# Optimization experiments

Hardware: AMD Instinct MI355X
Metric: run time of the kernel (lower is better)

Reference implementation:

```python
import jax, jax.numpy as jnp
import numpy as np


def _linear(x, w, b=None):
    # torch nn.Linear: y = x @ W^T + b, W has shape [out, in]
    y = jnp.einsum('...i,oi->...o', x, w)
    return y if b is None else y + b


def setup_inputs() -> dict:
    key = jax.random.key(0)
    ks = jax.random.split(key, 20)
    B, S = 2048, 128

    def w(k, out_d, in_d):
        bound = 1.0 / np.sqrt(in_d)
        return jax.random.uniform(k, (out_d, in_d), jnp.float32, -bound, bound)

    def bias(k, out_d, in_d):
        bound = 1.0 / np.sqrt(in_d)
        return jax.random.uniform(k, (out_d,), jnp.float32, -bound, bound)

    return {
        'x': jax.random.normal(ks[0], (B, S, 8), jnp.float32),
        'w_fm': w(ks[1], 16, 8),  'b_fm': bias(ks[2], 16, 8),
        'w_c1': w(ks[3], 16, 16), 'b_c1': bias(ks[4], 16, 16),
        'w_p1': w(ks[5], 12, 16), 'b_p1': bias(ks[6], 12, 16),
        'w_c2': w(ks[7], 8, 12),  'b_c2': bias(ks[8], 8, 12),
        'w_p2': w(ks[9], 4, 8),   'b_p2': bias(ks[10], 4, 8),
        'w_c3': w(ks[11], 4, 4),  'b_c3': bias(ks[12], 4, 4),
        'w_q': w(ks[13], 4, 4),
        'w_k': w(ks[14], 4, 4),
        'w_v': w(ks[15], 4, 4),
        'w_fc': w(ks[16], 1, 4),  'b_fc': bias(ks[17], 1, 4),
    }


def reference(x, w_fm, b_fm, w_c1, b_c1, w_p1, b_p1, w_c2, b_c2,
              w_p2, b_p2, w_c3, b_c3, w_q, w_k, w_v, w_fc, b_fc):
    EMBED_DIM = 4
    h = jnp.tanh(_linear(x, w_fm, b_fm))   # [B,S,16]
    h = jnp.tanh(_linear(h, w_c1, b_c1))   # [B,S,16]
    h = jnp.tanh(_linear(h, w_p1, b_p1))   # [B,S,12]
    h = jnp.tanh(_linear(h, w_c2, b_c2))   # [B,S,8]
    h = jnp.tanh(_linear(h, w_p2, b_p2))   # [B,S,4]
    h = jnp.tanh(_linear(h, w_c3, b_c3))   # [B,S,4]
    # self-attention over sequence axis
    q = _linear(h, w_q)                     # [B,S,4]
    k = _linear(h, w_k)
    v = _linear(h, w_v)
    scores = jnp.einsum('bqd,bkd->bqk', q, k) / np.sqrt(EMBED_DIM)
    attn = jax.nn.softmax(scores, axis=-1)  # [B,S,S]
    h = jnp.einsum('bqk,bkd->bqd', attn, v) # [B,S,4]
    out = _linear(h, w_fc, b_fc)            # [B,S,1]
    return jax.nn.sigmoid(out)
```

## Files before the change

### kernel.cpp

```cpp
#include <hip/hip_runtime.h>

#define DEV __device__ __forceinline__

typedef _Float16 h2 __attribute__((ext_vector_type(2)));
typedef float    f2 __attribute__((ext_vector_type(2)));

DEV float fast_rcp(float x) { return __builtin_amdgcn_rcpf(x); }

DEV float fexp2(float x) {
#if __has_builtin(__builtin_amdgcn_exp2f)
    return __builtin_amdgcn_exp2f(x);
#else
    float r; asm("v_exp_f32 %0, %1" : "=v"(r) : "v"(x)); return r;
#endif
}

DEV float dot2acc(h2 a, h2 b, float c) {
#if __has_builtin(__builtin_amdgcn_fdot2)
    return __builtin_amdgcn_fdot2(a, b, c, false);
#else
    return c + (float)a.x * (float)b.x + (float)a.y * (float)b.y;
#endif
}

DEV void pk_fma(f2& acc, f2 w2, f2 in2) {
    asm("v_pk_fma_f32 %0, %1, %2, %0" : "+v"(acc) : "s"(w2), "v"(in2));
}
DEV f2 pk_fma_z(f2 w2, f2 in2) {
    f2 d;
    asm("v_pk_fma_f32 %0, %1, %2, 0 op_sel_hi:[1,1,0]"
        : "=v"(d) : "s"(w2), "v"(in2));
    return d;
}
DEV void pk_fma_bcast(f2& acc, f2 e, f2 du) {
    asm("v_pk_fma_f32 %0, %1, %2, %0 op_sel:[0,0,0] op_sel_hi:[0,1,1]"
        : "+v"(acc) : "v"(e), "v"(du));
}

DEV float fast_tanh_pre(float t) {
    float e = fexp2(t);
    return 1.0f - 2.0f * fast_rcp(e + 1.0f);
}
DEV float fast_sigmoid(float x) {
    return fast_rcp(1.0f + fexp2(x * -1.442695041f));
}

#define TANH_K 2.885390082f

template <int IN, int OUT, bool TANH>
DEV void layer_pk(const float* __restrict__ w, const float* __restrict__ b,
                  float vK, const float (&in)[IN], float (&out)[OUT]) {
    static_assert(IN % 2 == 0, "IN must be even");
    f2 in2[IN / 2];
    #pragma unroll
    for (int ip = 0; ip < IN / 2; ++ip) in2[ip] = f2{in[2 * ip], in[2 * ip + 1]};
    #pragma unroll
    for (int o = 0; o < OUT; ++o) {
        f2 acc = pk_fma_z(*reinterpret_cast<const f2*>(w + o * IN), in2[0]);
        #pragma unroll
        for (int ip = 1; ip < IN / 2; ++ip)
            pk_fma(acc, *reinterpret_cast<const f2*>(w + o * IN + 2 * ip), in2[ip]);
        float s = acc.x + acc.y;
        if (TANH) {
            float bk = b[o] * vK;
            out[o] = fast_tanh_pre(fmaf(s, vK, bk));
        } else {
            out[o] = s;
        }
    }
}

__global__ __launch_bounds__(256)
void qcnn_fused_kernel(const float* __restrict__ x,
                       const float* __restrict__ w_fm, const float* __restrict__ b_fm,
                       const float* __restrict__ w_c1, const float* __restrict__ b_c1,
                       const float* __restrict__ w_p1, const float* __restrict__ b_p1,
                       const float* __restrict__ w_c2, const float* __restrict__ b_c2,
                       const float* __restrict__ w_p2, const float* __restrict__ b_p2,
                       const float* __restrict__ w_c3, const float* __restrict__ b_c3,
                       const float* __restrict__ w_q,  const float* __restrict__ w_k,
                       const float* __restrict__ w_v,
                       const float* __restrict__ w_fc, const float* __restrict__ b_fc,
                       float* __restrict__ out) {
    const int t     = threadIdx.x;
    const int bb    = t >> 7;
    const int tok   = t & 127;
    const int batch = blockIdx.x * 2 + bb;

    __shared__ uint4 kvbuf[2][128];

    const float vK = TANH_K;

    const float* xp = x + ((size_t)batch * 128 + tok) * 8;
    float4 x0 = *reinterpret_cast<const float4*>(xp);
    float4 x1 = *reinterpret_cast<const float4*>(xp + 4);
    float xin[8] = {x0.x, x0.y, x0.z, x0.w, x1.x, x1.y, x1.z, x1.w};

    float h1[16], h2a[16], h3[12], h4[8], h5[4], h6[4];
    layer_pk<8, 16, true>(w_fm, b_fm, vK, xin, h1);
    layer_pk<16, 16, true>(w_c1, b_c1, vK, h1, h2a);
    layer_pk<16, 12, true>(w_p1, b_p1, vK, h2a, h3);
    layer_pk<12, 8, true>(w_c2, b_c2, vK, h3, h4);
    layer_pk<8, 4, true>(w_p2, b_p2, vK, h4, h5);
    layer_pk<4, 4, true>(w_c3, b_c3, vK, h5, h6);

    float qv[4], kk[4];
    layer_pk<4, 4, false>(w_q, nullptr, vK, h6, qv);
    layer_pk<4, 4, false>(w_k, nullptr, vK, h6, kk);

    float wf[4];
    #pragma unroll
    for (int i = 0; i < 4; ++i)
        wf[i] = fmaf(w_fc[0], w_v[0 * 4 + i],
                fmaf(w_fc[1], w_v[1 * 4 + i],
                fmaf(w_fc[2], w_v[2 * 4 + i], w_fc[3] * w_v[3 * 4 + i])));
    float u = fmaf(wf[0], h6[0], fmaf(wf[1], h6[1], fmaf(wf[2], h6[2], wf[3] * h6[3])));

    h2 pk01 = {(_Float16)kk[0], (_Float16)kk[1]};
    h2 pk23 = {(_Float16)kk[2], (_Float16)kk[3]};
    uint4 ent;
    ent.x = __builtin_bit_cast(unsigned, pk01);
    ent.y = __builtin_bit_cast(unsigned, pk23);
    ent.z = __builtin_bit_cast(unsigned, 1.0f);
    ent.w = __builtin_bit_cast(unsigned, u);
    kvbuf[bb][tok] = ent;

    const float QS = 0.7213475204f;
    h2 q01 = {(_Float16)(qv[0] * QS), (_Float16)(qv[1] * QS)};
    h2 q23 = {(_Float16)(qv[2] * QS), (_Float16)(qv[3] * QS)};

    __syncthreads();

    unsigned q01u = __builtin_bit_cast(unsigned, q01);
    unsigned q23u = __builtin_bit_cast(unsigned, q23);
    unsigned q01o = __shfl_xor(q01u, 1);
    unsigned q23o = __shfl_xor(q23u, 1);
    const bool odd = (t & 1);
    h2 q01_r0 = __builtin_bit_cast(h2, odd ? q01o : q01u);
    h2 q23_r0 = __builtin_bit_cast(h2, odd ? q23o : q23u);
    h2 q01_r1 = __builtin_bit_cast(h2, odd ? q01u : q01o);
    h2 q23_r1 = __builtin_bit_cast(h2, odd ? q23u : q23o);

    const uint4* __restrict__ base = kvbuf[bb] + (odd ? 64 : 0);
    f2 acc0 = {0.f, 0.f};
    f2 acc1 = {0.f, 0.f};
    #pragma unroll 8
    for (int j = 0; j < 64; ++j) {
        uint4 c = base[j];
        h2 k01 = __builtin_bit_cast(h2, c.x);
        h2 k23 = __builtin_bit_cast(h2, c.y);
        f2 du;
        du.x = __builtin_bit_cast(float, c.z);
        du.y = __builtin_bit_cast(float, c.w);
        float s0 = dot2acc(q01_r0, k01, dot2acc(q23_r0, k23, 0.f));
        float s1 = dot2acc(q01_r1, k01, dot2acc(q23_r1, k23, 0.f));
        f2 e0; e0.x = fexp2(s0);
        f2 e1; e1.x = fexp2(s1);
        pk_fma_bcast(acc0, e0, du);
        pk_fma_bcast(acc1, e1, du);
    }

    f2 p0, p1;
    p0.x = __shfl_xor(acc0.x, 1);  p0.y = __shfl_xor(acc0.y, 1);
    p1.x = __shfl_xor(acc1.x, 1);  p1.y = __shfl_xor(acc1.y, 1);
    acc0 += p0;
    acc1 += p1;

    float dd = odd ? acc1.x : acc0.x;
    float uu = odd ? acc1.y : acc0.y;
    float z = fmaf(uu, fast_rcp(dd), b_fc[0]);
    out[(size_t)batch * 128 + tok] = fast_sigmoid(z);
}

extern "C" void kernel_launch(void* const* d_in, const int* in_sizes, int n_in,
                              void* d_out, int out_size, void* d_ws, size_t ws_size,
                              hipStream_t stream) {
    const float* x    = (const float*)d_in[0];
    const float* w_fm = (const float*)d_in[1];
    const float* b_fm = (const float*)d_in[2];
    const float* w_c1 = (const float*)d_in[3];
    const float* b_c1 = (const float*)d_in[4];
    const float* w_p1 = (const float*)d_in[5];
    const float* b_p1 = (const float*)d_in[6];
    const float* w_c2 = (const float*)d_in[7];
    const float* b_c2 = (const float*)d_in[8];
    const float* w_p2 = (const float*)d_in[9];
    const float* b_p2 = (const float*)d_in[10];
    const float* w_c3 = (const float*)d_in[11];
    const float* b_c3 = (const float*)d_in[12];
    const float* w_q  = (const float*)d_in[13];
    const float* w_k  = (const float*)d_in[14];
    const float* w_v  = (const float*)d_in[15];
    const float* w_fc = (const float*)d_in[16];
    const float* b_fc = (const float*)d_in[17];
    float* out = (float*)d_out;

    dim3 grid(1024);
    dim3 block(256);
    qcnn_fused_kernel<<<grid, block, 0, stream>>>(
        x, w_fm, b_fm, w_c1, b_c1, w_p1, b_p1, w_c2, b_c2,
        w_p2, b_p2, w_c3, b_c3, w_q, w_k, w_v, w_fc, b_fc, out);
}
```

Measured before the change: 20.23 us.

## Split each token's attention across two threads with 512-thread blocks

Doubles the block to 512 threads so two threads own each token, each scanning half of the 128 keys. Partial softmax sums are combined through shared memory and a second barrier, replacing the earlier approach where one thread scanned two interleaved query rows and combined them with lane shuffles. Layer activations are now kept as packed float2 arrays. The aim is more resident waves to hide latency, but both threads of a token recompute the full MLP, so per-token dense work doubles and a barrier is added.

```diff
diff --git a/kernel.cpp b/kernel.cpp
--- a/kernel.cpp
+++ b/kernel.cpp
@@ -49,28 +49,26 @@
 
 template <int IN, int OUT, bool TANH>
 DEV void layer_pk(const float* __restrict__ w, const float* __restrict__ b,
-                  float vK, const float (&in)[IN], float (&out)[OUT]) {
-    static_assert(IN % 2 == 0, "IN must be even");
-    f2 in2[IN / 2];
-    #pragma unroll
-    for (int ip = 0; ip < IN / 2; ++ip) in2[ip] = f2{in[2 * ip], in[2 * ip + 1]};
+                  float vK, const f2 (&in)[IN / 2], f2 (&out)[OUT / 2]) {
     #pragma unroll
     for (int o = 0; o < OUT; ++o) {
-        f2 acc = pk_fma_z(*reinterpret_cast<const f2*>(w + o * IN), in2[0]);
+        f2 acc = pk_fma_z(*reinterpret_cast<const f2*>(w + o * IN), in[0]);
         #pragma unroll
         for (int ip = 1; ip < IN / 2; ++ip)
-            pk_fma(acc, *reinterpret_cast<const f2*>(w + o * IN + 2 * ip), in2[ip]);
+            pk_fma(acc, *reinterpret_cast<const f2*>(w + o * IN + 2 * ip), in[ip]);
         float s = acc.x + acc.y;
+        float r;
         if (TANH) {
             float bk = b[o] * vK;
-            out[o] = fast_tanh_pre(fmaf(s, vK, bk));
+            r = fast_tanh_pre(fmaf(s, vK, bk));
         } else {
-            out[o] = s;
+            r = s;
         }
+        if (o & 1) out[o >> 1].y = r; else out[o >> 1].x = r;
     }
 }
 
-__global__ __launch_bounds__(256)
+__global__ __launch_bounds__(512, 8)
 void qcnn_fused_kernel(const float* __restrict__ x,
                        const float* __restrict__ w_fm, const float* __restrict__ b_fm,
                        const float* __restrict__ w_c1, const float* __restrict__ b_c1,
@@ -83,20 +81,23 @@
                        const float* __restrict__ w_fc, const float* __restrict__ b_fc,
                        float* __restrict__ out) {
     const int t     = threadIdx.x;
-    const int bb    = t >> 7;
-    const int tok   = t & 127;
-    const int batch = blockIdx.x * 2 + bb;
+    const int sub   = t >> 8;
+    const int tid   = t & 255;
+    const int tok   = tid & 127;
+    const int jh    = tid >> 7;
+    const int batch = blockIdx.x * 2 + sub;
 
     __shared__ uint4 kvbuf[2][128];
+    __shared__ f2    pp[2][128];
 
     const float vK = TANH_K;
 
     const float* xp = x + ((size_t)batch * 128 + tok) * 8;
     float4 x0 = *reinterpret_cast<const float4*>(xp);
     float4 x1 = *reinterpret_cast<const float4*>(xp + 4);
-    float xin[8] = {x0.x, x0.y, x0.z, x0.w, x1.x, x1.y, x1.z, x1.w};
+    f2 xin[4] = {f2{x0.x, x0.y}, f2{x0.z, x0.w}, f2{x1.x, x1.y}, f2{x1.z, x1.w}};
 
-    float h1[16], h2a[16], h3[12], h4[8], h5[4], h6[4];
+    f2 h1[8], h2a[8], h3[6], h4[4], h5[2], h6[2];
     layer_pk<8, 16, true>(w_fm, b_fm, vK, xin, h1);
     layer_pk<16, 16, true>(w_c1, b_c1, vK, h1, h2a);
     layer_pk<16, 12, true>(w_p1, b_p1, vK, h2a, h3);
@@ -104,46 +105,36 @@
     layer_pk<8, 4, true>(w_p2, b_p2, vK, h4, h5);
     layer_pk<4, 4, true>(w_c3, b_c3, vK, h5, h6);
 
-    float qv[4], kk[4];
-    layer_pk<4, 4, false>(w_q, nullptr, vK, h6, qv);
-    layer_pk<4, 4, false>(w_k, nullptr, vK, h6, kk);
+    f2 qv2[2];
+    layer_pk<4, 4, false>(w_q, nullptr, vK, h6, qv2);
+    const float QS = 0.7213475204f;
+    h2 q01 = {(_Float16)(qv2[0].x * QS), (_Float16)(qv2[0].y * QS)};
+    h2 q23 = {(_Float16)(qv2[1].x * QS), (_Float16)(qv2[1].y * QS)};
 
-    float wf[4];
-    #pragma unroll
-    for (int i = 0; i < 4; ++i)
-        wf[i] = fmaf(w_fc[0], w_v[0 * 4 + i],
-                fmaf(w_fc[1], w_v[1 * 4 + i],
-                fmaf(w_fc[2], w_v[2 * 4 + i], w_fc[3] * w_v[3 * 4 + i])));
-    float u = fmaf(wf[0], h6[0], fmaf(wf[1], h6[1], fmaf(wf[2], h6[2], wf[3] * h6[3])));
-
-    h2 pk01 = {(_Float16)kk[0], (_Float16)kk[1]};
-    h2 pk23 = {(_Float16)kk[2], (_Float16)kk[3]};
-    uint4 ent;
-    ent.x = __builtin_bit_cast(unsigned, pk01);
-    ent.y = __builtin_bit_cast(unsigned, pk23);
-    ent.z = __builtin_bit_cast(unsigned, 1.0f);
-    ent.w = __builtin_bit_cast(unsigned, u);
-    kvbuf[bb][tok] = ent;
-
-    const float QS = 0.7213475204f;
-    h2 q01 = {(_Float16)(qv[0] * QS), (_Float16)(qv[1] * QS)};
-    h2 q23 = {(_Float16)(qv[2] * QS), (_Float16)(qv[3] * QS)};
-
+    if (jh == 0) {
+        f2 kk2[2];
+        layer_pk<4, 4, false>(w_k, nullptr, vK, h6, kk2);
+        float wf[4];
+        #pragma unroll
+        for (int i = 0; i < 4; ++i)
+            wf[i] = fmaf(w_fc[0], w_v[0 * 4 + i],
+                    fmaf(w_fc[1], w_v[1 * 4 + i],
+                    fmaf(w_fc[2], w_v[2 * 4 + i], w_fc[3] * w_v[3 * 4 + i])));
+        float u = fmaf(wf[0], h6[0].x, fmaf(wf[1], h6[0].y,
+                  fmaf(wf[2], h6[1].x, wf[3] * h6[1].y)));
+        h2 pk01 = {(_Float16)kk2[0].x, (_Float16)kk2[0].y};
+        h2 pk23 = {(_Float16)kk2[1].x, (_Float16)kk2[1].y};
+        uint4 ent;
+        ent.x = __builtin_bit_cast(unsigned, pk01);
+        ent.y = __builtin_bit_cast(unsigned, pk23);
+        ent.z = __builtin_bit_cast(unsigned, 1.0f);
+        ent.w = __builtin_bit_cast(unsigned, u);
+        kvbuf[sub][tok] = ent;
+    }
     __syncthreads();
 
-    unsigned q01u = __builtin_bit_cast(unsigned, q01);
-    unsigned q23u = __builtin_bit_cast(unsigned, q23);
-    unsigned q01o = __shfl_xor(q01u, 1);
-    unsigned q23o = __shfl_xor(q23u, 1);
-    const bool odd = (t & 1);
-    h2 q01_r0 = __builtin_bit_cast(h2, odd ? q01o : q01u);
-    h2 q23_r0 = __builtin_bit_cast(h2, odd ? q23o : q23u);
-    h2 q01_r1 = __builtin_bit_cast(h2, odd ? q01u : q01o);
-    h2 q23_r1 = __builtin_bit_cast(h2, odd ? q23u : q23o);
-
-    const uint4* __restrict__ base = kvbuf[bb] + (odd ? 64 : 0);
-    f2 acc0 = {0.f, 0.f};
-    f2 acc1 = {0.f, 0.f};
+    const uint4* __restrict__ base = kvbuf[sub] + jh * 64;
+    f2 acc = {0.f, 0.f};
     #pragma unroll 8
     for (int j = 0; j < 64; ++j) {
         uint4 c = base[j];
@@ -152,24 +143,20 @@
         f2 du;
         du.x = __builtin_bit_cast(float, c.z);
         du.y = __builtin_bit_cast(float, c.w);
-        float s0 = dot2acc(q01_r0, k01, dot2acc(q23_r0, k23, 0.f));
-        float s1 = dot2acc(q01_r1, k01, dot2acc(q23_r1, k23, 0.f));
-        f2 e0; e0.x = fexp2(s0);
-        f2 e1; e1.x = fexp2(s1);
-        pk_fma_bcast(acc0, e0, du);
-        pk_fma_bcast(acc1, e1, du);
+        float s = dot2acc(q01, k01, dot2acc(q23, k23, 0.f));
+        f2 e; e.x = fexp2(s);
+        pk_fma_bcast(acc, e, du);
     }
 
-    f2 p0, p1;
-    p0.x = __shfl_xor(acc0.x, 1);  p0.y = __shfl_xor(acc0.y, 1);
-    p1.x = __shfl_xor(acc1.x, 1);  p1.y = __shfl_xor(acc1.y, 1);
-    acc0 += p0;
-    acc1 += p1;
+    if (jh == 1) pp[sub][tok] = acc;
+    __syncthreads();
 
-    float dd = odd ? acc1.x : acc0.x;
-    float uu = odd ? acc1.y : acc0.y;
-    float z = fmaf(uu, fast_rcp(dd), b_fc[0]);
-    out[(size_t)batch * 128 + tok] = fast_sigmoid(z);
+    if (jh == 0) {
+        f2 o = pp[sub][tok];
+        acc += o;
+        float z = fmaf(acc.y, fast_rcp(acc.x), b_fc[0]);
+        out[(size_t)batch * 128 + tok] = fast_sigmoid(z);
+    }
 }
 
 extern "C" void kernel_launch(void* const* d_in, const int* in_sizes, int n_in,
@@ -196,7 +183,7 @@
     float* out = (float*)d_out;
 
     dim3 grid(1024);
-    dim3 block(256);
+    dim3 block(512);
     qcnn_fused_kernel<<<grid, block, 0, stream>>>(
         x, w_fm, b_fm, w_c1, b_c1, w_p1, b_p1, w_c2, b_c2,
         w_p2, b_p2, w_c3, b_c3, w_q, w_k, w_v, w_fc, b_fc, out);
```

Result: slower. 26.97 us (+33.3%).
